# Kernel tuning notes

Measured on AMD Instinct MI355X. Metric: run time of the kernel, lower is better.

The kernel has to match this reference:

```python
import jax, jax.numpy as jnp
import numpy as np

T, H, E, I, TOP_K = 4096, 1024, 8, 2048, 2
EPS = 1e-05


def setup_inputs() -> dict:
    key = jax.random.key(0)
    ks = jax.random.split(key, 4)
    x = jax.random.normal(ks[0], (T, H), dtype=jnp.float32)
    scale = jnp.ones((H,), dtype=jnp.float32)
    gate_kernel = jax.random.normal(ks[1], (H, E), dtype=jnp.float32) * (1.0 / np.sqrt(H))
    gate_bias = jnp.zeros((E,), dtype=jnp.float32)
    mlp1_weight = jax.random.normal(ks[2], (E, H, 2 * I), dtype=jnp.float32) * (1.0 / np.sqrt(H))
    mlp1_bias = jnp.zeros((E, 2 * I), dtype=jnp.float32)
    mlp2_weight = jax.random.normal(ks[3], (E, I, H), dtype=jnp.float32) * (1.0 / np.sqrt(I))
    mlp2_bias = jnp.zeros((E, H), dtype=jnp.float32)
    return {"x": x, "scale": scale, "gate_kernel": gate_kernel, "gate_bias": gate_bias,
            "mlp1_weight": mlp1_weight, "mlp1_bias": mlp1_bias,
            "mlp2_weight": mlp2_weight, "mlp2_bias": mlp2_bias}


def _rmsnorm(x, scale):
    t = x.astype(jnp.float32)
    rms = jnp.sqrt(jnp.mean(t * t, axis=-1, keepdims=True) + EPS)
    return ((t / rms) * scale).astype(x.dtype)


def reference(x, scale, gate_kernel, gate_bias, mlp1_weight, mlp1_bias, mlp2_weight, mlp2_bias):
    normed = _rmsnorm(x, scale)                                   # [T, H]
    _ = normed @ gate_kernel + gate_bias                          # gate logits (unused: static routing)
    # dense per-token, all-expert MLP: [T,H] x [E,H,2I] -> [T,E,2I]
    hidden = jnp.einsum('th,ehi->tei', normed, mlp1_weight) + mlp1_bias
    gate = jnp.minimum(hidden[..., :I], 7.0)
    linear = jnp.clip(hidden[..., I:], -7.0, 7.0)
    activated = gate * jax.nn.sigmoid(1.702 * gate) * (linear + 1.0)
    expert_out = jnp.einsum('tei,eih->teh', activated, mlp2_weight) + mlp2_bias  # [T,E,H]
    # static uniform routing over the first TOP_K experts
    mix = jnp.where(jnp.arange(E) < TOP_K, 1.0 / TOP_K, 0.0).astype(x.dtype)     # [E]
    fused = jnp.einsum('teh,e->th', expert_out, mix)
    return x + fused
```

## Files before the change

kernel.cpp:

```cpp
#include <hip/hip_runtime.h>
#include <hip/hip_bf16.h>
#include <stdint.h>

#define T_DIM 4096
#define H_DIM 1024
#define I_DIM 2048

typedef __bf16 bf16x8 __attribute__((ext_vector_type(8)));
typedef float f32x4 __attribute__((ext_vector_type(4)));
typedef unsigned short ushort_t;
typedef unsigned short us4 __attribute__((ext_vector_type(4)));

__device__ __forceinline__ unsigned short f32_to_bf16(float f) {
  unsigned int u = __float_as_uint(f);
  u += 0x7fffu + ((u >> 16) & 1u);
  return (unsigned short)(u >> 16);
}

__device__ __forceinline__ void gload_lds16(const void* g, void* l) {
  __builtin_amdgcn_global_load_lds(
      (__attribute__((address_space(1))) void*)(uintptr_t)g,
      (__attribute__((address_space(3))) void*)(unsigned int)(uintptr_t)l,
      16, 0, 0);
}

__device__ __forceinline__ int swz(int L) { return L ^ (((L >> 7) & 7) << 4); }

#define S_BARRIER() asm volatile("s_barrier" ::: "memory")
#define WAITV(n) asm volatile("s_waitcnt vmcnt(" #n ")" ::: "memory")
#define IRFENCE() asm volatile("" ::: "memory")
#define MFMA16(acc, va, vb) \
  acc = __builtin_amdgcn_mfma_f32_16x16x32_bf16(va, vb, acc, 0, 0, 0)

__global__ __launch_bounds__(256) void k_rmsnorm_init(
    const float* __restrict__ x, const float* __restrict__ scale,
    const float* __restrict__ b2, ushort_t* __restrict__ normed,
    float* __restrict__ out) {
  const int row = blockIdx.x, tid = threadIdx.x;
  const float4 v = ((const float4*)(x + (size_t)row * H_DIM))[tid];
  float ss = v.x * v.x + v.y * v.y + v.z * v.z + v.w * v.w;
#pragma unroll
  for (int off = 32; off > 0; off >>= 1) ss += __shfl_xor(ss, off);
  __shared__ float wsum[4];
  if ((tid & 63) == 0) wsum[tid >> 6] = ss;
  __syncthreads();
  const float tot = wsum[0] + wsum[1] + wsum[2] + wsum[3];
  const float inv = rsqrtf(tot * (1.0f / H_DIM) + 1e-5f);
  const float4 sc = ((const float4*)scale)[tid];
  us4 o;
  o.x = f32_to_bf16(v.x * inv * sc.x);
  o.y = f32_to_bf16(v.y * inv * sc.y);
  o.z = f32_to_bf16(v.z * inv * sc.z);
  o.w = f32_to_bf16(v.w * inv * sc.w);
  ((us4*)(normed + (size_t)row * H_DIM))[tid] = o;
  const float4 b0 = ((const float4*)b2)[tid];
  const float4 b1 = ((const float4*)(b2 + H_DIM))[tid];
  float4 ov;
  ov.x = v.x + 0.5f * (b0.x + b1.x);
  ov.y = v.y + 0.5f * (b0.y + b1.y);
  ov.z = v.z + 0.5f * (b0.z + b1.z);
  ov.w = v.w + 0.5f * (b0.w + b1.w);
  ((float4*)(out + (size_t)row * H_DIM))[tid] = ov;
}

__global__ __launch_bounds__(256) void k_transpose_cvt(const float* __restrict__ src,
                                                       ushort_t* __restrict__ dst,
                                                       int R, int C) {
  __shared__ float tile[32][33];
  const size_t eoff = (size_t)blockIdx.z * (size_t)R * (size_t)C;
  src += eoff;
  dst += eoff;
  const int x0 = blockIdx.x * 32, y0 = blockIdx.y * 32;
  const int tx = threadIdx.x & 31, ty = threadIdx.x >> 5;
#pragma unroll
  for (int i = 0; i < 4; ++i)
    tile[ty + 8 * i][tx] = src[(size_t)(y0 + ty + 8 * i) * C + x0 + tx];
  __syncthreads();
#pragma unroll
  for (int i = 0; i < 4; ++i)
    dst[(size_t)(x0 + ty + 8 * i) * R + y0 + tx] = f32_to_bf16(tile[tx][ty + 8 * i]);
}

__global__ __launch_bounds__(512, 2) void k_gemm1_8ph(
    const ushort_t* __restrict__ normed, const ushort_t* __restrict__ w1T,
    const float* __restrict__ b1, ushort_t* __restrict__ act) {
  __shared__ __align__(16) ushort_t lds[2][4][8192];
  char* const ldsB = (char*)&lds[0][0][0];
  const int tid = threadIdx.x;
  const int wg = (blockIdx.x & 7) * 64 + (blockIdx.x >> 3);
  const int e = wg >> 8;
  const int rem = wg & 255;
  const int brow = (rem >> 4) * 256;
  const int bcol = (rem & 15) * 128;
  const int lane = tid & 63;
  const int wm = (tid >> 6) >> 1;
  const int wn = (tid >> 6) & 1;
  const int r16 = lane & 15, kh = lane >> 4;

  const ushort_t* aBase = normed + (size_t)brow * H_DIM;
  const ushort_t* gBase = w1T + ((size_t)e * 2 * I_DIM + bcol) * H_DIM;
  const ushort_t* lBase = gBase + (size_t)I_DIM * H_DIM;

  f32x4 accg[4][4], accl[4][4];
  const f32x4 zf = {0.f, 0.f, 0.f, 0.f};
#pragma unroll
  for (int m = 0; m < 4; ++m)
#pragma unroll
    for (int n = 0; n < 4; ++n) { accg[m][n] = zf; accl[m][n] = zf; }

  int srow[2], scolb[2];
#pragma unroll
  for (int j = 0; j < 2; ++j) {
    const int u = swz((j * 512 + tid) * 16);
    srow[j] = u >> 6;
    scolb[j] = (u & 63) >> 1;
  }
  const int ldst0 = (tid & ~63) * 16;

  const ushort_t* pA0 = aBase + (size_t)srow[0] * H_DIM + scolb[0];
  const ushort_t* pA1 = aBase + (size_t)srow[1] * H_DIM + scolb[1];
  const ushort_t* pG = gBase + (size_t)srow[0] * H_DIM + scolb[0];
  const ushort_t* pL = lBase + (size_t)(srow[1] - 128) * H_DIM + scolb[1];

  int aoffV[2][4], boffV[2][4];
#pragma unroll
  for (int bq = 0; bq < 2; ++bq) {
#pragma unroll
    for (int m = 0; m < 4; ++m)
      aoffV[bq][m] = bq * 65536 + swz((wm * 64 + m * 16 + r16) * 64 + kh * 16);
#pragma unroll
    for (int n = 0; n < 4; ++n)
      boffV[bq][n] = bq * 65536 + 16384 + swz((wn * 64 + n * 16 + r16) * 64 + kh * 16);
  }

  auto stageA = [&](int buf, int ksub) {
    gload_lds16(pA0 + ksub * 32, ldsB + buf * 65536 + ksub * 32768 + ldst0);
    gload_lds16(pA1 + ksub * 32, ldsB + buf * 65536 + ksub * 32768 + 8192 + ldst0);
  };
  auto stageB = [&](int buf, int ksub) {
    gload_lds16(pG + ksub * 32, ldsB + buf * 65536 + ksub * 32768 + 16384 + ldst0);
    gload_lds16(pL + ksub * 32, ldsB + buf * 65536 + ksub * 32768 + 16384 + 8192 + ldst0);
  };
  auto rdA = [&](int buf, int ksub, int m) -> bf16x8 {
    return *(const bf16x8*)(ldsB + aoffV[buf][m] + ksub * 32768);
  };
  auto rdBg = [&](int buf, int ksub, int n) -> bf16x8 {
    return *(const bf16x8*)(ldsB + boffV[buf][n] + ksub * 32768);
  };
  auto rdBl = [&](int buf, int ksub, int n) -> bf16x8 {
    return *(const bf16x8*)(ldsB + boffV[buf][n] + ksub * 32768 + 8192);
  };

#define G1_ADV() \
  { pA0 += 64; pA1 += 64; pG += 64; pL += 64; }

#define G1_HALF(CUR, NXT, KS)                                                 \
  {                                                                           \
    _Pragma("unroll") for (int m = 0; m < 4; ++m) a[m] = rdA(CUR, KS, m);     \
    _Pragma("unroll") for (int n = 0; n < 4; ++n) b[n] = rdBg(CUR, KS, n);    \
    stageA(NXT, KS);                                                          \
    stageB(NXT, KS);                                                          \
    __builtin_amdgcn_s_setprio(1);                                            \
    _Pragma("unroll") for (int m = 0; m < 4; ++m)                             \
        _Pragma("unroll") for (int n = 0; n < 4; ++n)                         \
            MFMA16(accg[m][n], a[m], b[n]);                                   \
    __builtin_amdgcn_s_setprio(0);                                            \
    _Pragma("unroll") for (int n = 0; n < 4; ++n) b[n] = rdBl(CUR, KS, n);    \
    __builtin_amdgcn_s_setprio(1);                                            \
    _Pragma("unroll") for (int m = 0; m < 4; ++m)                             \
        _Pragma("unroll") for (int n = 0; n < 4; ++n)                         \
            MFMA16(accl[m][n], a[m], b[n]);                                   \
    __builtin_amdgcn_s_setprio(0);                                            \
    WAITV(4);                                                                 \
    S_BARRIER();                                                              \
  }

#define G1_TILE(CUR, NXT)  \
  { G1_HALF(CUR, NXT, 0); G1_HALF(CUR, NXT, 1); G1_ADV(); }

  stageA(0, 0); stageB(0, 0); IRFENCE();
  stageA(0, 1); stageB(0, 1);
  G1_ADV();
  WAITV(4);
  S_BARRIER();

  bf16x8 a[4], b[4];
#pragma unroll 1
  for (int it = 0; it < 7; ++it) {
    G1_TILE(0, 1);
    G1_TILE(1, 0);
  }
  G1_TILE(0, 1);

  {
#pragma unroll
    for (int m = 0; m < 4; ++m) a[m] = rdA(1, 0, m);
#pragma unroll
    for (int n = 0; n < 4; ++n) b[n] = rdBg(1, 0, n);
#pragma unroll
    for (int m = 0; m < 4; ++m)
#pragma unroll
      for (int n = 0; n < 4; ++n) MFMA16(accg[m][n], a[m], b[n]);
#pragma unroll
    for (int n = 0; n < 4; ++n) b[n] = rdBl(1, 0, n);
#pragma unroll
    for (int m = 0; m < 4; ++m)
#pragma unroll
      for (int n = 0; n < 4; ++n) MFMA16(accl[m][n], a[m], b[n]);
    WAITV(0);
    S_BARRIER();
#pragma unroll
    for (int m = 0; m < 4; ++m) a[m] = rdA(1, 1, m);
#pragma unroll
    for (int n = 0; n < 4; ++n) b[n] = rdBg(1, 1, n);
#pragma unroll
    for (int m = 0; m < 4; ++m)
#pragma unroll
      for (int n = 0; n < 4; ++n) MFMA16(accg[m][n], a[m], b[n]);
#pragma unroll
    for (int n = 0; n < 4; ++n) b[n] = rdBl(1, 1, n);
#pragma unroll
    for (int m = 0; m < 4; ++m)
#pragma unroll
      for (int n = 0; n < 4; ++n) MFMA16(accl[m][n], a[m], b[n]);
  }
#undef G1_HALF
#undef G1_TILE
#undef G1_ADV

  const float* b1e = b1 + (size_t)e * 2 * I_DIM;
#pragma unroll
  for (int m = 0; m < 4; ++m)
#pragma unroll
    for (int n = 0; n < 4; ++n) {
      const int gcol = bcol + wn * 64 + n * 16 + r16;
      const float bgb = b1e[gcol];
      const float blb = b1e[I_DIM + gcol];
#pragma unroll
      for (int rr = 0; rr < 4; ++rr) {
        const int grow = brow + wm * 64 + m * 16 + kh * 4 + rr;
        const float hg = accg[m][n][rr] + bgb;
        const float hl = accl[m][n][rr] + blb;
        const float g = fminf(hg, 7.f);
        const float l = fminf(fmaxf(hl, -7.f), 7.f);
        const float s = 1.f / (1.f + __expf(-1.702f * g));
        const float av = g * s * (l + 1.f);
        act[((size_t)e * T_DIM + grow) * I_DIM + gcol] = f32_to_bf16(av);
      }
    }
}

__global__ __launch_bounds__(512, 2) void k_gemm2_8ph(
    const ushort_t* __restrict__ act, const ushort_t* __restrict__ w2T,
    float* __restrict__ out) {
  __shared__ __align__(16) ushort_t lds[2][2][12288];
  char* const ldsB = (char*)&lds[0][0][0];
  const int tid = threadIdx.x;
  const int wg = (blockIdx.x & 7) * 32 + (blockIdx.x >> 3);
  const int e = wg >> 7;
  const int tileid = wg & 127;
  const int brow = (tileid >> 3) * 256;
  const int bcol = (tileid & 7) * 128;
  const int lane = tid & 63;
  const int wm = (tid >> 6) >> 1;
  const int wn = (tid >> 6) & 1;
  const int r16 = lane & 15, kh = lane >> 4;

  const ushort_t* aBase = act + ((size_t)e * T_DIM + brow) * I_DIM;
  const ushort_t* bBase = w2T + ((size_t)e * H_DIM + bcol) * I_DIM;

  f32x4 acc[4][4];
  const f32x4 zf = {0.f, 0.f, 0.f, 0.f};
#pragma unroll
  for (int m = 0; m < 4; ++m)
#pragma unroll
    for (int n = 0; n < 4; ++n) acc[m][n] = zf;

  int srow[2], scolb[2];
#pragma unroll
  for (int j = 0; j < 2; ++j) {
    const int u = swz((j * 512 + tid) * 16);
    srow[j] = u >> 6;
    scolb[j] = (u & 63) >> 1;
  }
  const int ldst0 = (tid & ~63) * 16;

  const ushort_t* pA0 = aBase + (size_t)srow[0] * I_DIM + scolb[0];
  const ushort_t* pA1 = aBase + (size_t)srow[1] * I_DIM + scolb[1];
  const ushort_t* pB = bBase + (size_t)srow[0] * I_DIM + scolb[0];

  int aoffV[2][4], boffV[2][4];
#pragma unroll
  for (int bq = 0; bq < 2; ++bq) {
#pragma unroll
    for (int m = 0; m < 4; ++m)
      aoffV[bq][m] = bq * 49152 + swz((wm * 64 + m * 16 + r16) * 64 + kh * 16);
#pragma unroll
    for (int n = 0; n < 4; ++n)
      boffV[bq][n] = bq * 49152 + 16384 + swz((wn * 64 + n * 16 + r16) * 64 + kh * 16);
  }

  auto stageA = [&](int buf, int ksub) {
    gload_lds16(pA0 + ksub * 32, ldsB + buf * 49152 + ksub * 24576 + ldst0);
    gload_lds16(pA1 + ksub * 32, ldsB + buf * 49152 + ksub * 24576 + 8192 + ldst0);
  };
  auto stageB = [&](int buf, int ksub) {
    gload_lds16(pB + ksub * 32, ldsB + buf * 49152 + ksub * 24576 + 16384 + ldst0);
  };
  auto rdA = [&](int buf, int ksub, int m) -> bf16x8 {
    return *(const bf16x8*)(ldsB + aoffV[buf][m] + ksub * 24576);
  };
  auto rdB = [&](int buf, int ksub, int n) -> bf16x8 {
    return *(const bf16x8*)(ldsB + boffV[buf][n] + ksub * 24576);
  };

#define G2_ADV() \
  { pA0 += 64; pA1 += 64; pB += 64; }

#define G2_HALF(CUR, NXT, KS)                                                 \
  {                                                                           \
    _Pragma("unroll") for (int m = 0; m < 4; ++m) a[m] = rdA(CUR, KS, m);     \
    _Pragma("unroll") for (int n = 0; n < 4; ++n) b[n] = rdB(CUR, KS, n);     \
    stageA(NXT, KS);                                                          \
    stageB(NXT, KS);                                                          \
    __builtin_amdgcn_s_setprio(1);                                            \
    _Pragma("unroll") for (int m = 0; m < 4; ++m)                             \
        _Pragma("unroll") for (int n = 0; n < 4; ++n)                         \
            MFMA16(acc[m][n], a[m], b[n]);                                    \
    __builtin_amdgcn_s_setprio(0);                                            \
    WAITV(3);                                                                 \
    S_BARRIER();                                                              \
  }

#define G2_TILE(CUR, NXT)  \
  { G2_HALF(CUR, NXT, 0); G2_HALF(CUR, NXT, 1); G2_ADV(); }

  stageA(0, 0); stageB(0, 0); IRFENCE();
  stageA(0, 1); stageB(0, 1);
  G2_ADV();
  WAITV(3);
  S_BARRIER();

  bf16x8 a[4], b[4];
#pragma unroll 1
  for (int it = 0; it < 15; ++it) {
    G2_TILE(0, 1);
    G2_TILE(1, 0);
  }
  G2_TILE(0, 1);

  {
#pragma unroll
    for (int m = 0; m < 4; ++m) a[m] = rdA(1, 0, m);
#pragma unroll
    for (int n = 0; n < 4; ++n) b[n] = rdB(1, 0, n);
#pragma unroll
    for (int m = 0; m < 4; ++m)
#pragma unroll
      for (int n = 0; n < 4; ++n) MFMA16(acc[m][n], a[m], b[n]);
    WAITV(0);
    S_BARRIER();
#pragma unroll
    for (int m = 0; m < 4; ++m) a[m] = rdA(1, 1, m);
#pragma unroll
    for (int n = 0; n < 4; ++n) b[n] = rdB(1, 1, n);
#pragma unroll
    for (int m = 0; m < 4; ++m)
#pragma unroll
      for (int n = 0; n < 4; ++n) MFMA16(acc[m][n], a[m], b[n]);
  }
#undef G2_HALF
#undef G2_TILE
#undef G2_ADV

#pragma unroll
  for (int m = 0; m < 4; ++m)
#pragma unroll
    for (int n = 0; n < 4; ++n) {
      const int gcol = bcol + wn * 64 + n * 16 + r16;
#pragma unroll
      for (int rr = 0; rr < 4; ++rr) {
        const int grow = brow + wm * 64 + m * 16 + kh * 4 + rr;
        atomicAdd(&out[(size_t)grow * H_DIM + gcol], 0.5f * acc[m][n][rr]);
      }
    }
}

extern "C" void kernel_launch(void* const* d_in, const int* in_sizes, int n_in,
                              void* d_out, int out_size, void* d_ws, size_t ws_size,
                              hipStream_t stream) {
  const float* x = (const float*)d_in[0];
  const float* scale = (const float*)d_in[1];
  const float* w1 = (const float*)d_in[4];
  const float* b1 = (const float*)d_in[5];
  const float* w2 = (const float*)d_in[6];
  const float* b2 = (const float*)d_in[7];
  float* out = (float*)d_out;

  ushort_t* ws = (ushort_t*)d_ws;
  ushort_t* normed = ws;
  ushort_t* w1T = normed + (size_t)T_DIM * H_DIM;
  ushort_t* w2T = w1T + (size_t)2 * 2 * I_DIM * H_DIM;
  ushort_t* actb = w2T + (size_t)2 * H_DIM * I_DIM;

  k_rmsnorm_init<<<dim3(T_DIM), 256, 0, stream>>>(x, scale, b2, normed, out);
  k_transpose_cvt<<<dim3(2 * I_DIM / 32, H_DIM / 32, 2), 256, 0, stream>>>(
      w1, w1T, H_DIM, 2 * I_DIM);
  k_transpose_cvt<<<dim3(H_DIM / 32, I_DIM / 32, 2), 256, 0, stream>>>(
      w2, w2T, I_DIM, H_DIM);
  k_gemm1_8ph<<<dim3(512), 512, 0, stream>>>(normed, w1T, b1, actb);
  k_gemm2_8ph<<<dim3(256), 512, 0, stream>>>(actb, w2T, out);
}
```

Before: 149.2 us.

## Reshape gemm1 wave tiling to 2x4 and interleave LDS reads with MFMA phases

Changes gemm1's wave layout from 4x2 waves with 64x64 sub-tiles to 2x4 waves each covering 128 rows by 32 gate and 32 linear columns. It reorganizes each K tile into four MFMA quadrant phases, with LDS reads and global-to-LDS staging interleaved between them. Explicit lgkmcnt waits, sched_barriers and extra s_barriers pin the ordering. The goal is to hide LDS read latency behind MFMA and change the A/B fragment reuse ratio, at the cost of more barriers and a different register footprint.

```diff
diff --git a/kernel.cpp b/kernel.cpp
--- a/kernel.cpp
+++ b/kernel.cpp
@@ -28,6 +28,9 @@
 
 #define S_BARRIER() asm volatile("s_barrier" ::: "memory")
 #define WAITV(n) asm volatile("s_waitcnt vmcnt(" #n ")" ::: "memory")
+#define LGKM0() asm volatile("s_waitcnt lgkmcnt(0)" ::: "memory")
+#define LGKM8() asm volatile("s_waitcnt lgkmcnt(8)" ::: "memory")
+#define SCHEDB() __builtin_amdgcn_sched_barrier(0)
 #define IRFENCE() asm volatile("" ::: "memory")
 #define MFMA16(acc, va, vb) \
   acc = __builtin_amdgcn_mfma_f32_16x16x32_bf16(va, vb, acc, 0, 0, 0)
@@ -81,7 +84,7 @@
     dst[(size_t)(x0 + ty + 8 * i) * R + y0 + tx] = f32_to_bf16(tile[tx][ty + 8 * i]);
 }
 
-__global__ __launch_bounds__(512, 2) void k_gemm1_8ph(
+__global__ __launch_bounds__(512, 2) void k_gemm1(
     const ushort_t* __restrict__ normed, const ushort_t* __restrict__ w1T,
     const float* __restrict__ b1, ushort_t* __restrict__ act) {
   __shared__ __align__(16) ushort_t lds[2][4][8192];
@@ -93,20 +96,20 @@
   const int brow = (rem >> 4) * 256;
   const int bcol = (rem & 15) * 128;
   const int lane = tid & 63;
-  const int wm = (tid >> 6) >> 1;
-  const int wn = (tid >> 6) & 1;
+  const int wid = tid >> 6;
+  const int wm = wid >> 2;
+  const int wn = wid & 3;
   const int r16 = lane & 15, kh = lane >> 4;
 
-  const ushort_t* aBase = normed + (size_t)brow * H_DIM;
   const ushort_t* gBase = w1T + ((size_t)e * 2 * I_DIM + bcol) * H_DIM;
   const ushort_t* lBase = gBase + (size_t)I_DIM * H_DIM;
 
-  f32x4 accg[4][4], accl[4][4];
+  f32x4 accg[8][2], accl[8][2];
   const f32x4 zf = {0.f, 0.f, 0.f, 0.f};
 #pragma unroll
-  for (int m = 0; m < 4; ++m)
-#pragma unroll
-    for (int n = 0; n < 4; ++n) { accg[m][n] = zf; accl[m][n] = zf; }
+  for (int m = 0; m < 8; ++m)
+#pragma unroll
+    for (int n = 0; n < 2; ++n) { accg[m][n] = zf; accl[m][n] = zf; }
 
   int srow[2], scolb[2];
 #pragma unroll
@@ -117,66 +120,98 @@
   }
   const int ldst0 = (tid & ~63) * 16;
 
-  const ushort_t* pA0 = aBase + (size_t)srow[0] * H_DIM + scolb[0];
-  const ushort_t* pA1 = aBase + (size_t)srow[1] * H_DIM + scolb[1];
+  const ushort_t* pA0 = normed + (size_t)(brow + srow[0]) * H_DIM + scolb[0];
+  const ushort_t* pA1 = normed + (size_t)(brow + srow[1]) * H_DIM + scolb[1];
   const ushort_t* pG = gBase + (size_t)srow[0] * H_DIM + scolb[0];
   const ushort_t* pL = lBase + (size_t)(srow[1] - 128) * H_DIM + scolb[1];
 
-  int aoffV[2][4], boffV[2][4];
-#pragma unroll
-  for (int bq = 0; bq < 2; ++bq) {
-#pragma unroll
-    for (int m = 0; m < 4; ++m)
-      aoffV[bq][m] = bq * 65536 + swz((wm * 64 + m * 16 + r16) * 64 + kh * 16);
-#pragma unroll
-    for (int n = 0; n < 4; ++n)
-      boffV[bq][n] = bq * 65536 + 16384 + swz((wn * 64 + n * 16 + r16) * 64 + kh * 16);
-  }
-
-  auto stageA = [&](int buf, int ksub) {
-    gload_lds16(pA0 + ksub * 32, ldsB + buf * 65536 + ksub * 32768 + ldst0);
-    gload_lds16(pA1 + ksub * 32, ldsB + buf * 65536 + ksub * 32768 + 8192 + ldst0);
-  };
-  auto stageB = [&](int buf, int ksub) {
-    gload_lds16(pG + ksub * 32, ldsB + buf * 65536 + ksub * 32768 + 16384 + ldst0);
-    gload_lds16(pL + ksub * 32, ldsB + buf * 65536 + ksub * 32768 + 16384 + 8192 + ldst0);
-  };
-  auto rdA = [&](int buf, int ksub, int m) -> bf16x8 {
-    return *(const bf16x8*)(ldsB + aoffV[buf][m] + ksub * 32768);
-  };
-  auto rdBg = [&](int buf, int ksub, int n) -> bf16x8 {
-    return *(const bf16x8*)(ldsB + boffV[buf][n] + ksub * 32768);
-  };
-  auto rdBl = [&](int buf, int ksub, int n) -> bf16x8 {
-    return *(const bf16x8*)(ldsB + boffV[buf][n] + ksub * 32768 + 8192);
-  };
+  int abase[2], bbase[2];
+  {
+    const int ab = wm * 8192 + swz(r16 * 64 + kh * 16);
+    const int bb = 16384 + swz((wn * 32 + r16) * 64 + kh * 16);
+#pragma unroll
+    for (int bq = 0; bq < 2; ++bq) {
+      abase[bq] = bq * 65536 + ab;
+      bbase[bq] = bq * 65536 + bb;
+    }
+  }
+
+  auto stageA = [&](int buf, int ks) {
+    gload_lds16(pA0 + ks * 32, ldsB + buf * 65536 + ks * 32768 + ldst0);
+    gload_lds16(pA1 + ks * 32, ldsB + buf * 65536 + ks * 32768 + 8192 + ldst0);
+  };
+  auto stageB = [&](int buf, int ks) {
+    gload_lds16(pG + ks * 32, ldsB + buf * 65536 + ks * 32768 + 16384 + ldst0);
+    gload_lds16(pL + ks * 32, ldsB + buf * 65536 + ks * 32768 + 16384 + 8192 + ldst0);
+  };
+
+  bf16x8 a[8], bg0[2], bl0[2], bg1[2], bl1[2];
+
+#define RD_A(C, KS)                                                           \
+  _Pragma("unroll") for (int m = 0; m < 8; ++m)                               \
+      a[m] = *(const bf16x8*)(ldsB + abase[C] + (KS) * 32768 + m * 1024);
+#define RD_B(C, KS, BG, BL)                                                   \
+  _Pragma("unroll") for (int n = 0; n < 2; ++n) {                             \
+    BG[n] = *(const bf16x8*)(ldsB + bbase[C] + (KS) * 32768 + n * 1024);      \
+    BL[n] = *(const bf16x8*)(ldsB + bbase[C] + (KS) * 32768 + 8192 + n * 1024);\
+  }
+#define MFMA_Q(MQ, BG, BL)                                                    \
+  _Pragma("unroll") for (int mm = 0; mm < 4; ++mm)                            \
+      _Pragma("unroll") for (int n = 0; n < 2; ++n) {                         \
+    MFMA16(accg[(MQ) * 4 + mm][n], a[(MQ) * 4 + mm], BG[n]);                  \
+    MFMA16(accl[(MQ) * 4 + mm][n], a[(MQ) * 4 + mm], BL[n]);                  \
+  }
 
 #define G1_ADV() \
   { pA0 += 64; pA1 += 64; pG += 64; pL += 64; }
 
-#define G1_HALF(CUR, NXT, KS)                                                 \
-  {                                                                           \
-    _Pragma("unroll") for (int m = 0; m < 4; ++m) a[m] = rdA(CUR, KS, m);     \
-    _Pragma("unroll") for (int n = 0; n < 4; ++n) b[n] = rdBg(CUR, KS, n);    \
-    stageA(NXT, KS);                                                          \
-    stageB(NXT, KS);                                                          \
+#define G1_TILE(C, N)                                                         \
+  {                          \
+    RD_A(C, 0);                                                               \
+    RD_B(C, 0, bg0, bl0);                                                     \
+    stageA(N, 0);                                                             \
+    stageB(N, 0);                                                             \
+    LGKM8();                                                                  \
+    S_BARRIER();                                                              \
+    LGKM0();                                                                  \
+    SCHEDB();                                                                 \
     __builtin_amdgcn_s_setprio(1);                                            \
-    _Pragma("unroll") for (int m = 0; m < 4; ++m)                             \
-        _Pragma("unroll") for (int n = 0; n < 4; ++n)                         \
-            MFMA16(accg[m][n], a[m], b[n]);                                   \
+    MFMA_Q(0, bg0, bl0);                                                      \
     __builtin_amdgcn_s_setprio(0);                                            \
-    _Pragma("unroll") for (int n = 0; n < 4; ++n) b[n] = rdBl(CUR, KS, n);    \
+    WAITV(4);         \
+    S_BARRIER();                                                              \
+    SCHEDB();                                                                 \
+                              \
+    RD_B(C, 1, bg1, bl1);                                                     \
+    stageA(N, 1);                                                             \
+    stageB(N, 1);                                                             \
+    S_BARRIER();                                                              \
+    LGKM0();                                                                  \
+    SCHEDB();                                                                 \
     __builtin_amdgcn_s_setprio(1);                                            \
-    _Pragma("unroll") for (int m = 0; m < 4; ++m)                             \
-        _Pragma("unroll") for (int n = 0; n < 4; ++n)                         \
-            MFMA16(accl[m][n], a[m], b[n]);                                   \
+    MFMA_Q(1, bg0, bl0);                                                      \
     __builtin_amdgcn_s_setprio(0);                                            \
-    WAITV(4);                                                                 \
-    S_BARRIER();                                                              \
-  }
-
-#define G1_TILE(CUR, NXT)  \
-  { G1_HALF(CUR, NXT, 0); G1_HALF(CUR, NXT, 1); G1_ADV(); }
+    S_BARRIER();                                                              \
+    SCHEDB();                                                                 \
+                                             \
+    RD_A(C, 1);                                                               \
+    S_BARRIER();                                                              \
+    LGKM0();                                                                  \
+    SCHEDB();                                                                 \
+    __builtin_amdgcn_s_setprio(1);                                            \
+    MFMA_Q(0, bg1, bl1);                                                      \
+    __builtin_amdgcn_s_setprio(0);                                            \
+    S_BARRIER();                                                              \
+    SCHEDB();                                                                 \
+                                  \
+    __builtin_amdgcn_s_setprio(1);                                            \
+    MFMA_Q(1, bg1, bl1);                                                      \
+    __builtin_amdgcn_s_setprio(0);                                            \
+    WAITV(4);                             \
+    S_BARRIER();                                                              \
+    SCHEDB();                                                                 \
+    G1_ADV();                                                                 \
+  }
 
   stageA(0, 0); stageB(0, 0); IRFENCE();
   stageA(0, 1); stageB(0, 1);
@@ -184,7 +219,6 @@
   WAITV(4);
   S_BARRIER();
 
-  bf16x8 a[4], b[4];
 #pragma unroll 1
   for (int it = 0; it < 7; ++it) {
     G1_TILE(0, 1);
@@ -193,52 +227,34 @@
   G1_TILE(0, 1);
 
   {
-#pragma unroll
-    for (int m = 0; m < 4; ++m) a[m] = rdA(1, 0, m);
-#pragma unroll
-    for (int n = 0; n < 4; ++n) b[n] = rdBg(1, 0, n);
-#pragma unroll
-    for (int m = 0; m < 4; ++m)
-#pragma unroll
-      for (int n = 0; n < 4; ++n) MFMA16(accg[m][n], a[m], b[n]);
-#pragma unroll
-    for (int n = 0; n < 4; ++n) b[n] = rdBl(1, 0, n);
-#pragma unroll
-    for (int m = 0; m < 4; ++m)
-#pragma unroll
-      for (int n = 0; n < 4; ++n) MFMA16(accl[m][n], a[m], b[n]);
+    RD_A(1, 0);
+    RD_B(1, 0, bg0, bl0);
+    MFMA_Q(0, bg0, bl0);
     WAITV(0);
     S_BARRIER();
-#pragma unroll
-    for (int m = 0; m < 4; ++m) a[m] = rdA(1, 1, m);
-#pragma unroll
-    for (int n = 0; n < 4; ++n) b[n] = rdBg(1, 1, n);
-#pragma unroll
-    for (int m = 0; m < 4; ++m)
-#pragma unroll
-      for (int n = 0; n < 4; ++n) MFMA16(accg[m][n], a[m], b[n]);
-#pragma unroll
-    for (int n = 0; n < 4; ++n) b[n] = rdBl(1, 1, n);
-#pragma unroll
-    for (int m = 0; m < 4; ++m)
-#pragma unroll
-      for (int n = 0; n < 4; ++n) MFMA16(accl[m][n], a[m], b[n]);
-  }
-#undef G1_HALF
+    RD_B(1, 1, bg1, bl1);
+    MFMA_Q(1, bg0, bl0);
+    RD_A(1, 1);
+    MFMA_Q(0, bg1, bl1);
+    MFMA_Q(1, bg1, bl1);
+  }
 #undef G1_TILE
 #undef G1_ADV
+#undef RD_A
+#undef RD_B
+#undef MFMA_Q
 
   const float* b1e = b1 + (size_t)e * 2 * I_DIM;
 #pragma unroll
-  for (int m = 0; m < 4; ++m)
-#pragma unroll
-    for (int n = 0; n < 4; ++n) {
-      const int gcol = bcol + wn * 64 + n * 16 + r16;
+  for (int m = 0; m < 8; ++m)
+#pragma unroll
+    for (int n = 0; n < 2; ++n) {
+      const int gcol = bcol + wn * 32 + n * 16 + r16;
       const float bgb = b1e[gcol];
       const float blb = b1e[I_DIM + gcol];
 #pragma unroll
       for (int rr = 0; rr < 4; ++rr) {
-        const int grow = brow + wm * 64 + m * 16 + kh * 4 + rr;
+        const int grow = brow + wm * 128 + m * 16 + kh * 4 + rr;
         const float hg = accg[m][n][rr] + bgb;
         const float hl = accl[m][n][rr] + blb;
         const float g = fminf(hg, 7.f);
@@ -250,7 +266,7 @@
     }
 }
 
-__global__ __launch_bounds__(512, 2) void k_gemm2_8ph(
+__global__ __launch_bounds__(512, 2) void k_gemm2(
     const ushort_t* __restrict__ act, const ushort_t* __restrict__ w2T,
     float* __restrict__ out) {
   __shared__ __align__(16) ushort_t lds[2][2][12288];
@@ -408,6 +424,6 @@
       w1, w1T, H_DIM, 2 * I_DIM);
   k_transpose_cvt<<<dim3(H_DIM / 32, I_DIM / 32, 2), 256, 0, stream>>>(
       w2, w2T, I_DIM, H_DIM);
-  k_gemm1_8ph<<<dim3(512), 512, 0, stream>>>(normed, w1T, b1, actb);
-  k_gemm2_8ph<<<dim3(256), 512, 0, stream>>>(actb, w2T, out);
-}
+  k_gemm1<<<dim3(512), 512, 0, stream>>>(normed, w1T, b1, actb);
+  k_gemm2<<<dim3(256), 512, 0, stream>>>(actb, w2T, out);
+}
```

New measurement: 158.7 us. +6.4%, slower.
